# Kernel optimization log

Measured on AMD Instinct MI355X. Metric: run time of the kernel, lower is better.

The kernel has to match this reference:

```python
import jax, jax.numpy as jnp
import numpy as np

B, NVEC, DIM, HEADS, DH, M, ITERS, DEPTH, NCLASS, KER = 8, 4096, 512, 8, 64, 256, 6, 2, 10, 33
INNER = HEADS * DH


def _ln(x, g, b, eps=1e-5):
    mu = x.mean(-1, keepdims=True)
    var = ((x - mu) ** 2).mean(-1, keepdims=True)
    return (x - mu) * jax.lax.rsqrt(var + eps) * g + b


def _mp_pinv(x, iters=ITERS):
    # Moore-Penrose pseudo-inverse via Newton-Schulz iterations (lucidrains).
    # x: [b, h, m, m]
    abs_x = jnp.abs(x)
    col = abs_x.sum(-1).max(-1)  # [b, h]
    row = abs_x.sum(-2).max(-1)  # [b, h]
    z = jnp.swapaxes(x, -1, -2) / (col * row)[..., None, None]
    I = jnp.eye(x.shape[-1], dtype=x.dtype)
    for _ in range(iters):
        xz = x @ z
        z = 0.25 * z @ (13.0 * I - xz @ (15.0 * I - xz @ (7.0 * I - xz)))
    return z


def _nystrom_attn(x, qkv_w, out_w, out_b, conv_w):
    b, n, _ = x.shape
    qkv = x @ qkv_w  # [b, n, 3*inner]
    q, k, v = jnp.split(qkv, 3, axis=-1)
    to_h = lambda t: t.reshape(b, n, HEADS, DH).transpose(0, 2, 1, 3)  # [b,h,n,dh]
    q, k, v = to_h(q), to_h(k), to_h(v)
    q = q * (DH ** -0.5)

    l = n // M  # tokens per landmark segment (n divisible by M)
    q_l = q.reshape(b, HEADS, M, l, DH).mean(3)  # [b,h,M,dh]
    k_l = k.reshape(b, HEADS, M, l, DH).mean(3)

    attn1 = jax.nn.softmax(jnp.einsum('bhnd,bhmd->bhnm', q, k_l), axis=-1)    # [b,h,n,M]
    attn2 = jax.nn.softmax(jnp.einsum('bhmd,bhld->bhml', q_l, k_l), axis=-1)  # [b,h,M,M]
    attn3 = jax.nn.softmax(jnp.einsum('bhmd,bhnd->bhmn', q_l, k), axis=-1)    # [b,h,M,n]

    out = (attn1 @ _mp_pinv(attn2)) @ (attn3 @ v)  # [b,h,n,dh]

    # residual depthwise conv over sequence dim (kernel 33, groups=heads, no bias)
    out = out + jax.lax.conv_general_dilated(
        v, conv_w, (1, 1), [(KER // 2, KER // 2), (0, 0)],
        dimension_numbers=('NCHW', 'OIHW', 'NCHW'), feature_group_count=HEADS)

    out = out.transpose(0, 2, 1, 3).reshape(b, n, INNER)
    return out @ out_w + out_b


def setup_inputs():
    key = jax.random.key(0)
    ks = jax.random.split(key, 12)
    s = 0.02
    f32 = jnp.float32
    return {
        'x': jax.random.normal(ks[0], (B, NVEC, 2), f32),
        'lin_w': jax.random.normal(ks[1], (2, DIM), f32) * s,
        'lin_b': jnp.zeros((DIM,), f32),
        'ln1_g': jnp.ones((DEPTH, DIM), f32),
        'ln1_b': jnp.zeros((DEPTH, DIM), f32),
        'qkv_w': jax.random.normal(ks[2], (DEPTH, DIM, 3 * INNER), f32) * s,
        'out_w': jax.random.normal(ks[3], (DEPTH, INNER, DIM), f32) * s,
        'out_b': jnp.zeros((DEPTH, DIM), f32),
        'conv_w': jax.random.normal(ks[4], (DEPTH, HEADS, 1, KER, 1), f32) * s,
        'ln2_g': jnp.ones((DEPTH, DIM), f32),
        'ln2_b': jnp.zeros((DEPTH, DIM), f32),
        'ff1_w': jax.random.normal(ks[5], (DEPTH, DIM, 4 * DIM), f32) * s,
        'ff1_b': jnp.zeros((DEPTH, 4 * DIM), f32),
        'ff2_w': jax.random.normal(ks[6], (DEPTH, 4 * DIM, DIM), f32) * s,
        'ff2_b': jnp.zeros((DEPTH, DIM), f32),
        'final_w': jax.random.normal(ks[7], (NVEC * DIM, NCLASS), f32) * s,
        'final_b': jnp.zeros((NCLASS,), f32),
    }


def reference(x, lin_w, lin_b, ln1_g, ln1_b, qkv_w, out_w, out_b, conv_w,
              ln2_g, ln2_b, ff1_w, ff1_b, ff2_w, ff2_b, final_w, final_b):
    h = x @ lin_w + lin_b  # [B, NVEC, DIM]
    for i in range(DEPTH):
        h = h + _nystrom_attn(_ln(h, ln1_g[i], ln1_b[i]), qkv_w[i], out_w[i], out_b[i], conv_w[i])
        z = _ln(h, ln2_g[i], ln2_b[i])
        h = h + (jax.nn.gelu(z @ ff1_w[i] + ff1_b[i]) @ ff2_w[i] + ff2_b[i])
    return h.reshape(h.shape[0], -1) @ final_w + final_b  # [B, NCLASS]
```

## Files before the change

### kernel.cpp

```cpp
#include <hip/hip_runtime.h>
#include <hip/hip_bf16.h>

#define BB_ 8
#define NVEC 4096
#define DIM 512
#define HEADS 8
#define DH 64
#define MM_ 256
#define ITERS 6
#define DEPTH 2
#define NCLASS 10
#define KER 33
#define INNER 512
#define LSEG 16

typedef long long ll;
typedef __bf16 bh16;
typedef __attribute__((ext_vector_type(8))) __bf16 bf16x8;
typedef __attribute__((ext_vector_type(4))) float f32x4;

template<int WR, int WC, bool TRB, bool GELU_ACT, bool RESID, bool BF16OUT, bool DUAL>
__global__ void __launch_bounds__(256)
mgemm_k(const bh16* __restrict__ A, const bh16* __restrict__ B,
        const float* __restrict__ bias, void* __restrict__ Cv, void* __restrict__ C2v,
        int K, int lda, int ldb, int ldc,
        int BI, ll sAo, ll sAi, ll sBo, ll sBi, ll sCo, ll sCi,
        float alpha, float diagv)
{
    constexpr int BM = WR * 64, BN = WC * 64;
    const int bz = blockIdx.z;
    const int bo = bz / BI, bi = bz % BI;
    const bh16* Ab = A + bo * sAo + (ll)bi * sAi;
    const bh16* Bb = B + bo * sBo + (ll)bi * sBi;
    const ll coff = bo * sCo + (ll)bi * sCi;
    const int m0 = blockIdx.y * BM;
    const int n0 = blockIdx.x * BN;
    const int tid = threadIdx.x;
    const int lane = tid & 63;
    const int wave = tid >> 6;
    const int wr = wave / WC, wc = wave % WC;

    __shared__ bh16 Al[BM * 32];
    __shared__ bh16 Bl[BN * 32];

    f32x4 acc[4][4];
#pragma unroll
    for (int i = 0; i < 4; ++i)
#pragma unroll
        for (int j = 0; j < 4; ++j) acc[i][j] = (f32x4){0.f, 0.f, 0.f, 0.f};

    const int srow = tid >> 2;
    const int ssl  = tid & 3;

    const int rsel  = ((lane & 15) >> 1) & 3;
    const int kslot = lane >> 4;

    for (int k0 = 0; k0 < K; k0 += 32) {
        __syncthreads();
#pragma unroll
        for (int i = 0; i < BM / 64; ++i) {
            int row = i * 64 + srow;
            int sl = ssl ^ ((row >> 1) & 3);
            bf16x8 v = *(const bf16x8*)(Ab + (ll)(m0 + row) * lda + k0 + ssl * 8);
            *(bf16x8*)(Al + row * 32 + sl * 8) = v;
        }
        if (!TRB) {
#pragma unroll
            for (int i = 0; i < BN / 64; ++i) {
                int row = i * 64 + srow;
                int sl = ssl ^ ((row >> 1) & 3);
                bf16x8 v = *(const bf16x8*)(Bb + (ll)(n0 + row) * ldb + k0 + ssl * 8);
                *(bf16x8*)(Bl + row * 32 + sl * 8) = v;
            }
        } else {
            const int bk = tid >> 3;
            const int nb0 = (tid & 7) * (BN / 8);
#pragma unroll
            for (int v8 = 0; v8 < BN / 64; ++v8) {
                int nb = nb0 + v8 * 8;
                bf16x8 v = *(const bf16x8*)(Bb + (ll)(k0 + bk) * ldb + n0 + nb);
#pragma unroll
                for (int j = 0; j < 8; ++j) {
                    int n = nb + j;
                    int sl = (bk >> 3) ^ ((n >> 1) & 3);
                    Bl[n * 32 + sl * 8 + (bk & 7)] = v[j];
                }
            }
        }
        __syncthreads();

        bf16x8 af[4], bfr[4];
#pragma unroll
        for (int mi = 0; mi < 4; ++mi) {
            int row = wr * 64 + mi * 16 + (lane & 15);
            af[mi] = *(const bf16x8*)(Al + row * 32 + (kslot ^ rsel) * 8);
        }
#pragma unroll
        for (int ni = 0; ni < 4; ++ni) {
            int row = wc * 64 + ni * 16 + (lane & 15);
            bfr[ni] = *(const bf16x8*)(Bl + row * 32 + (kslot ^ rsel) * 8);
        }
#pragma unroll
        for (int mi = 0; mi < 4; ++mi)
#pragma unroll
            for (int ni = 0; ni < 4; ++ni)
                acc[mi][ni] = __builtin_amdgcn_mfma_f32_16x16x32_bf16(
                    af[mi], bfr[ni], acc[mi][ni], 0, 0, 0);
    }

#pragma unroll
    for (int mi = 0; mi < 4; ++mi) {
#pragma unroll
        for (int ni = 0; ni < 4; ++ni) {
            const int colg = n0 + wc * 64 + ni * 16 + (lane & 15);
            const float bia = (!DUAL && bias) ? bias[colg] : 0.f;
#pragma unroll
            for (int r = 0; r < 4; ++r) {
                const int rowg = m0 + wr * 64 + mi * 16 + (lane >> 4) * 4 + r;
                const float a = acc[mi][ni][r];
                const ll off = coff + (ll)rowg * ldc + colg;
                if (DUAL) {
                    ((bh16*)Cv)[off] = (bh16)a;
                    float w = ((rowg == colg) ? diagv : 0.f) - a;
                    ((bh16*)C2v)[off] = (bh16)w;
                } else {
                    float v = alpha * a + bia;
                    if (diagv != 0.f && rowg == colg) v += diagv;
                    if (GELU_ACT) {
                        float t = tanhf(0.7978845608f * (v + 0.044715f * v * v * v));
                        v = 0.5f * v * (1.0f + t);
                    }
                    if (BF16OUT) {
                        ((bh16*)Cv)[off] = (bh16)v;
                    } else {
                        float* p = (float*)Cv + off;
                        float o = v;
                        if (RESID) o += *p;
                        *p = o;
                    }
                }
            }
        }
    }
}

template<int WR, int WC, bool TRB, bool G, bool R, bool BO, bool D>
static inline void mg(hipStream_t s, int M, int N, int K,
                      const bh16* A, int lda, const bh16* B, int ldb,
                      void* C, int ldc, void* C2, const float* bias,
                      int batch, int BI,
                      ll sAo, ll sAi, ll sBo, ll sBi, ll sCo, ll sCi,
                      float alpha, float diagv)
{
    dim3 grid(N / (WC * 64), M / (WR * 64), batch);
    hipLaunchKernelGGL((mgemm_k<WR, WC, TRB, G, R, BO, D>), grid, dim3(256), 0, s,
                       A, B, bias, C, C2, K, lda, ldb, ldc, BI,
                       sAo, sAi, sBo, sBi, sCo, sCi, alpha, diagv);
}

__global__ void embed_k(const float* __restrict__ x, const float* __restrict__ w,
                        const float* __restrict__ b, float* __restrict__ h)
{
    ll idx = (ll)blockIdx.x * 256 + threadIdx.x;
    int d = (int)(idx & 511);
    ll bn = idx >> 9;
    h[idx] = x[bn * 2] * w[d] + x[bn * 2 + 1] * w[512 + d] + b[d];
}

__global__ void __launch_bounds__(256)
ln_k(const float* __restrict__ X, const float* __restrict__ g,
     const float* __restrict__ bta, bh16* __restrict__ Y)
{
    const ll row = blockIdx.x;
    const float* x = X + row * 512;
    bh16* y = Y + row * 512;
    const int tid = threadIdx.x;
    float v0 = x[tid], v1 = x[tid + 256];
    float s = v0 + v1;
    float q = v0 * v0 + v1 * v1;
    __shared__ float sred[8];
    for (int o = 32; o; o >>= 1) { s += __shfl_down(s, o); q += __shfl_down(q, o); }
    const int lane = tid & 63, w = tid >> 6;
    if (lane == 0) { sred[w] = s; sred[4 + w] = q; }
    __syncthreads();
    float ssum = sred[0] + sred[1] + sred[2] + sred[3];
    float qsum = sred[4] + sred[5] + sred[6] + sred[7];
    float mu = ssum * (1.0f / 512.0f);
    float var = qsum * (1.0f / 512.0f) - mu * mu;
    float r = rsqrtf(var + 1e-5f);
    y[tid] = (bh16)((v0 - mu) * r * g[tid] + bta[tid]);
    y[tid + 256] = (bh16)((v1 - mu) * r * g[tid + 256] + bta[tid + 256]);
}

__global__ void cvtT_k(const float* __restrict__ in, bh16* __restrict__ outp, int C, int R)
{
    int idx = blockIdx.x * 256 + threadIdx.x;
    int c = idx % C, rg = idx / C;
    bf16x8 o;
#pragma unroll
    for (int j = 0; j < 8; ++j) o[j] = (bh16)in[(ll)(rg * 8 + j) * C + c];
    *(bf16x8*)(outp + (ll)c * R + rg * 8) = o;
}

__global__ void landmarks_k(const bh16* __restrict__ qkv,
                            bh16* __restrict__ qlb, bh16* __restrict__ klb)
{
    int idx = blockIdx.x * 256 + threadIdx.x;
    int d = idx & 63;
    int m = (idx >> 6) & 255;
    int h = (idx >> 14) & 7;
    int b = idx >> 17;
    const bh16* base = qkv + (ll)b * (NVEC * 1536) + (ll)(m * LSEG) * 1536 + h * 64 + d;
    float sq = 0.f, sk = 0.f;
#pragma unroll
    for (int l = 0; l < LSEG; ++l) {
        sq += (float)base[(ll)l * 1536];
        sk += (float)base[(ll)l * 1536 + 512];
    }
    ll o = (ll)(b * 8 + h) * 16384 + m * 64 + d;
    qlb[o] = (bh16)(sq * (0.0625f * 0.125f));
    klb[o] = (bh16)(sk * 0.0625f);
}

__global__ void wbt_k(const bh16* __restrict__ wb, bh16* __restrict__ wbt)
{
    int idx = blockIdx.x * 256 + threadIdx.x;
    int d = idx & 63, kg = (idx >> 6) & 31, bhh = idx >> 11;
    const bh16* p = wb + (ll)bhh * 16384 + kg * 8 * 64 + d;
    bf16x8 o;
#pragma unroll
    for (int j = 0; j < 8; ++j) o[j] = p[j * 64];
    *(bf16x8*)(wbt + (ll)bhh * 16384 + d * 256 + kg * 8) = o;
}

__global__ void a3vred_k(const float* __restrict__ part, bh16* __restrict__ outp)
{
    int idx = blockIdx.x * 256 + threadIdx.x;
    int smp = idx >> 17;
    int rest = idx & 131071;
    int h = rest >> 14, o = rest & 16383;
    const float* p = part + (ll)smp * 1048576 + (ll)h * 131072 + o;
    float s = 0.f;
#pragma unroll
    for (int j = 0; j < 8; ++j) s += p[j * 16384];
    outp[(ll)(smp * 8 + h) * 16384 + o] = (bh16)s;
}

__global__ void __launch_bounds__(256)
conv_k(const bh16* __restrict__ qkv, const float* __restrict__ cw,
       bh16* __restrict__ convo)
{
    int idx = blockIdx.x * 256 + threadIdx.x;
    int c8 = idx & 63;
    int ng = (idx >> 6) & 1023;
    int b  = idx >> 16;
    const int n0 = ng * 4;
    const int h = c8 >> 3;
    const bh16* v = qkv + (ll)b * (NVEC * 1536) + 1024 + c8 * 8;

    float wreg[KER];
#pragma unroll
    for (int k = 0; k < KER; ++k) wreg[k] = cw[h * KER + k];

    float acc[4][8];
#pragma unroll
    for (int t = 0; t < 4; ++t)
#pragma unroll
        for (int e = 0; e < 8; ++e) acc[t][e] = 0.f;

#pragma unroll
    for (int m = 0; m < 36; ++m) {
        int nn = n0 + m - (KER / 2);
        bf16x8 vv = {};
        if ((unsigned)nn < (unsigned)NVEC)
            vv = *(const bf16x8*)(v + (ll)nn * 1536);
#pragma unroll
        for (int t = 0; t < 4; ++t) {
            constexpr int KMAX = KER - 1;
            int k = m - t;
            if (k >= 0 && k <= KMAX) {
                float wk = wreg[k];
#pragma unroll
                for (int e = 0; e < 8; ++e)
                    acc[t][e] = fmaf((float)vv[e], wk, acc[t][e]);
            }
        }
    }

    bh16* o = convo + (ll)b * (NVEC * 512) + (ll)n0 * 512 + c8 * 8;
#pragma unroll
    for (int t = 0; t < 4; ++t) {
        bf16x8 ov;
#pragma unroll
        for (int e = 0; e < 8; ++e) ov[e] = (bh16)acc[t][e];
        *(bf16x8*)(o + (ll)t * 512) = ov;
    }
}

__device__ __forceinline__ float blkmax(float m, float* red, int tid)
{
#pragma unroll
    for (int o = 32; o; o >>= 1) m = fmaxf(m, __shfl_down(m, o));
    if ((tid & 63) == 0) red[tid >> 6] = m;
    __syncthreads();
    m = fmaxf(fmaxf(red[0], red[1]), fmaxf(red[2], red[3]));
    __syncthreads();
    return m;
}
__device__ __forceinline__ float blksum(float s, float* red, int tid)
{
#pragma unroll
    for (int o = 32; o; o >>= 1) s += __shfl_down(s, o);
    if ((tid & 63) == 0) red[tid >> 6] = s;
    __syncthreads();
    s = red[0] + red[1] + red[2] + red[3];
    __syncthreads();
    return s;
}

__global__ void __launch_bounds__(256)
softmax_bf_k(bh16* __restrict__ X, int L)
{
    const ll row = blockIdx.x;
    bh16* x = X + row * (ll)L;
    const int tid = threadIdx.x;
    __shared__ float red[4];
    float v[16];
    bf16x8 a = *(const bf16x8*)(x + tid * 8);
    bf16x8 b = *(const bf16x8*)(x + 2048 + tid * 8);
#pragma unroll
    for (int j = 0; j < 8; ++j) { v[j] = (float)a[j]; v[8 + j] = (float)b[j]; }
    float m = -1e30f;
#pragma unroll
    for (int j = 0; j < 16; ++j) m = fmaxf(m, v[j]);
    m = blkmax(m, red, tid);
    float s = 0.f;
#pragma unroll
    for (int j = 0; j < 16; ++j) { v[j] = __expf(v[j] - m); s += v[j]; }
    s = blksum(s, red, tid);
    float inv = 1.0f / s;
    bf16x8 oa, ob;
#pragma unroll
    for (int j = 0; j < 8; ++j) { oa[j] = (bh16)(v[j] * inv); ob[j] = (bh16)(v[8 + j] * inv); }
    *(bf16x8*)(x + tid * 8) = oa;
    *(bf16x8*)(x + 2048 + tid * 8) = ob;
}

__global__ void __launch_bounds__(256)
softmax256_k(bh16* __restrict__ X)
{
    const int tid = threadIdx.x;
    const ll row = (ll)blockIdx.x * 8 + (tid >> 5);
    const int l = tid & 31;
    bh16* x = X + row * 256 + l * 8;
    bf16x8 a = *(const bf16x8*)x;
    float v[8];
#pragma unroll
    for (int j = 0; j < 8; ++j) v[j] = (float)a[j];
    float m = -1e30f;
#pragma unroll
    for (int j = 0; j < 8; ++j) m = fmaxf(m, v[j]);
#pragma unroll
    for (int o = 16; o; o >>= 1) m = fmaxf(m, __shfl_xor(m, o, 32));
    float s = 0.f;
#pragma unroll
    for (int j = 0; j < 8; ++j) { v[j] = __expf(v[j] - m); s += v[j]; }
#pragma unroll
    for (int o = 16; o; o >>= 1) s += __shfl_xor(s, o, 32);
    float inv = 1.0f / s;
    bf16x8 ov;
#pragma unroll
    for (int j = 0; j < 8; ++j) ov[j] = (bh16)(v[j] * inv);
    *(bf16x8*)x = ov;
}

__global__ void __launch_bounds__(256)
pinv_init_k(const bh16* __restrict__ X, bh16* __restrict__ Z)
{
    const ll bh = blockIdx.x;
    const bh16* x = X + bh * 65536;
    bh16* z = Z + bh * 65536;
    const int tid = threadIdx.x;
    float rs = 0.f, cs = 0.f;
    for (int j = 0; j < 256; ++j) {
        rs += fabsf((float)x[tid * 256 + j]);
        cs += fabsf((float)x[j * 256 + tid]);
    }
    __shared__ float rbuf[256], cbuf[256];
    rbuf[tid] = rs; cbuf[tid] = cs;
    __syncthreads();
    for (int o = 128; o; o >>= 1) {
        if (tid < o) {
            rbuf[tid] = fmaxf(rbuf[tid], rbuf[tid + o]);
            cbuf[tid] = fmaxf(cbuf[tid], cbuf[tid + o]);
        }
        __syncthreads();
    }
    float inv = 1.0f / (rbuf[0] * cbuf[0]);
    for (int e = tid; e < 65536; e += 256) {
        int i = e >> 8, j = e & 255;
        z[e] = (bh16)((float)x[j * 256 + i] * inv);
    }
}

__global__ void final_init_k(const float* __restrict__ fb, float* __restrict__ out)
{
    int i = threadIdx.x;
    if (i < BB_ * NCLASS) out[i] = fb[i % NCLASS];
}

__global__ void __launch_bounds__(256)
final_gemv_k(const float* __restrict__ hbuf, const float* __restrict__ w,
             float* __restrict__ out)
{
    const int b = blockIdx.y;
    const int chunk = blockIdx.x;
    const int tid = threadIdx.x;
    const float* hrow = hbuf + (ll)b * (NVEC * DIM);
    float pc[NCLASS] = {};
    const int k0 = chunk * 8192;
    for (int e = 0; e < 32; ++e) {
        int k = k0 + e * 256 + tid;
        float hv = hrow[k];
        const float* wr = w + (ll)k * NCLASS;
#pragma unroll
        for (int c = 0; c < NCLASS; ++c) pc[c] += hv * wr[c];
    }
    __shared__ float red[256];
    for (int c = 0; c < NCLASS; ++c) {
        red[tid] = pc[c];
        __syncthreads();
        for (int o = 128; o; o >>= 1) {
            if (tid < o) red[tid] += red[tid + o];
            __syncthreads();
        }
        if (tid == 0) atomicAdd(out + b * NCLASS + c, red[0]);
        __syncthreads();
    }
}

extern "C" void kernel_launch(void* const* d_in, const int* in_sizes, int n_in,
                              void* d_out, int out_size, void* d_ws, size_t ws_size,
                              hipStream_t stream)
{
    const float* x      = (const float*)d_in[0];
    const float* lin_w  = (const float*)d_in[1];
    const float* lin_b  = (const float*)d_in[2];
    const float* ln1_g  = (const float*)d_in[3];
    const float* ln1_b  = (const float*)d_in[4];
    const float* qkv_w  = (const float*)d_in[5];
    const float* out_w  = (const float*)d_in[6];
    const float* out_b  = (const float*)d_in[7];
    const float* conv_w = (const float*)d_in[8];
    const float* ln2_g  = (const float*)d_in[9];
    const float* ln2_b  = (const float*)d_in[10];
    const float* ff1_w  = (const float*)d_in[11];
    const float* ff1_b  = (const float*)d_in[12];
    const float* ff2_w  = (const float*)d_in[13];
    const float* ff2_b  = (const float*)d_in[14];
    const float* final_w = (const float*)d_in[15];
    const float* final_b = (const float*)d_in[16];
    float* out = (float*)d_out;
    float* ws  = (float*)d_ws;

    float* H    = ws;
    bh16*  QKV  = (bh16*)(ws + 16777216);
    float* P    = ws + 41943040;
    bh16*  qlbf = (bh16*)(ws + 52428800);
    bh16*  klbf = (bh16*)(ws + 52953088);
    bh16*  A3Vb = (bh16*)(ws + 53477376);
    bh16*  WBb  = (bh16*)(ws + 54001664);
    bh16*  WBT  = (bh16*)(ws + 54525952);
    bh16*  WQT  = (bh16*)(ws + 55050240);
    bh16*  WOT  = (bh16*)(ws + 55443456);
    bh16*  F1WT = (bh16*)(ws + 55574528);
    bh16*  F2WT = (bh16*)(ws + 56098816);
    if (ws_size < 56623104ULL * 4) return;

    bh16*  XLNall = (bh16*)P;
    bh16*  ATT3c  = (bh16*)P;
    float* A3Vp   = P + 8388608;
    bh16*  CONVa  = (bh16*)P;
    bh16*  Xbf = (bh16*)P;
    bh16*  Z0  = (bh16*)(P + 2097152);
    bh16*  Z1  = (bh16*)(P + 4194304);
    bh16*  T1  = (bh16*)(P + 6291456);
    bh16*  T2  = (bh16*)(P + 8388608);
    bh16*  ATT1c  = (bh16*)P;
    bh16*  AOUTc  = (bh16*)(P + 8388608);
    bh16*  XLNc   = (bh16*)P;
    bh16*  HIDc   = (bh16*)(P + 2097152);

    const ll SMP = (ll)NVEC * 1536;

    hipLaunchKernelGGL(embed_k, dim3(65536), dim3(256), 0, stream, x, lin_w, lin_b, H);

    for (int i = 0; i < DEPTH; ++i) {
        const float* wq  = qkv_w + (ll)i * 512 * 1536;
        const float* wo  = out_w + (ll)i * 512 * 512;
        const float* bo  = out_b + (ll)i * 512;
        const float* cw  = conv_w + (ll)i * HEADS * KER;
        const float* g1  = ln1_g + (ll)i * 512;
        const float* b1  = ln1_b + (ll)i * 512;
        const float* g2  = ln2_g + (ll)i * 512;
        const float* b2  = ln2_b + (ll)i * 512;
        const float* f1w = ff1_w + (ll)i * 512 * 2048;
        const float* f1b = ff1_b + (ll)i * 2048;
        const float* f2w = ff2_w + (ll)i * 2048 * 512;
        const float* f2b = ff2_b + (ll)i * 512;

        hipLaunchKernelGGL(cvtT_k, dim3(384), dim3(256), 0, stream, wq, WQT, 1536, 512);
        hipLaunchKernelGGL(cvtT_k, dim3(128), dim3(256), 0, stream, wo, WOT, 512, 512);
        hipLaunchKernelGGL(cvtT_k, dim3(512), dim3(256), 0, stream, f1w, F1WT, 2048, 512);
        hipLaunchKernelGGL(cvtT_k, dim3(512), dim3(256), 0, stream, f2w, F2WT, 512, 2048);

        hipLaunchKernelGGL(ln_k, dim3(32768), dim3(256), 0, stream, H, g1, b1, XLNall);
        mg<2,2,0,0,0,1,0>(stream, 32768, 1536, 512, XLNall, 512, WQT, 512,
            QKV, 1536, nullptr, nullptr, 1, 1, 0,0, 0,0, 0,0, 1.f, 0.f);

        hipLaunchKernelGGL(landmarks_k, dim3(4096), dim3(256), 0, stream, QKV, qlbf, klbf);

        for (int c = 0; c < 4; ++c) {
            const bh16* qkvc = QKV + (ll)c * 2 * SMP;
            mg<2,2,0,0,0,1,0>(stream, 256, 4096, 64,
                qlbf + (ll)c * 262144, 64, qkvc + 512, 1536,
                ATT3c, 4096, nullptr, nullptr, 16, 8,
                131072, 16384, SMP, 64, 8388608LL, 1048576, 1.f, 0.f);
            hipLaunchKernelGGL(softmax_bf_k, dim3(4096), dim3(256), 0, stream, ATT3c, 4096);
            for (int s = 0; s < 2; ++s) {
                mg<4,1,1,0,0,0,0>(stream, 256, 64, 512,
                    ATT3c + (ll)s * 8 * 1048576, 4096, qkvc + (ll)s * SMP + 1024, 1536,
                    A3Vp + (ll)s * 1048576, 64, nullptr, nullptr, 64, 8,
                    1048576, 512, 64, 512LL * 1536, 131072, 16384, 1.f, 0.f);
            }
            hipLaunchKernelGGL(a3vred_k, dim3(1024), dim3(256), 0, stream,
                               A3Vp, A3Vb + (ll)c * 2 * 131072);
        }

        hipLaunchKernelGGL(conv_k, dim3(2048), dim3(256), 0, stream, QKV, cw, CONVa);
        mg<2,2,0,0,1,0,0>(stream, 32768, 512, 512, CONVa, 512, WOT, 512,
            H, 512, nullptr, nullptr, 1, 1, 0,0, 0,0, 0,0, 1.f, 0.f);

        mg<2,2,0,0,0,1,0>(stream, 256, 256, 64, qlbf, 64, klbf, 64,
            Xbf, 256, nullptr, nullptr, 64, 64, 0, 16384, 0, 16384, 0, 65536, 1.f, 0.f);
        hipLaunchKernelGGL(softmax256_k, dim3(2048), dim3(256), 0, stream, Xbf);
        hipLaunchKernelGGL(pinv_init_k, dim3(64), dim3(256), 0, stream, Xbf, Z0);
        bh16* zc = Z0; bh16* zn = Z1;
        for (int it = 0; it < ITERS; ++it) {
            mg<2,2,1,0,0,1,1>(stream, 256, 256, 256, Xbf, 256, zc, 256,
                T1, 256, T2, nullptr, 64, 64, 0, 65536, 0, 65536, 0, 65536, 1.f, 7.f);
            mg<2,2,1,0,0,1,0>(stream, 256, 256, 256, T1, 256, T2, 256,
                zn, 256, nullptr, nullptr, 64, 64, 0, 65536, 0, 65536, 0, 65536, -1.f, 15.f);
            mg<2,2,1,0,0,1,0>(stream, 256, 256, 256, T1, 256, zn, 256,
                T2, 256, nullptr, nullptr, 64, 64, 0, 65536, 0, 65536, 0, 65536, -1.f, 13.f);
            mg<2,2,1,0,0,1,0>(stream, 256, 256, 256, zc, 256, T2, 256,
                zn, 256, nullptr, nullptr, 64, 64, 0, 65536, 0, 65536, 0, 65536, 0.25f, 0.f);
            bh16* t = zc; zc = zn; zn = t;
        }
        mg<4,1,1,0,0,1,0>(stream, 256, 64, 256, zc, 256, A3Vb, 64,
            WBb, 64, nullptr, nullptr, 64, 64, 0, 65536, 0, 16384, 0, 16384, 1.f, 0.f);
        hipLaunchKernelGGL(wbt_k, dim3(512), dim3(256), 0, stream, WBb, WBT);

        for (int c = 0; c < 4; ++c) {
            const bh16* qkvc = QKV + (ll)c * 2 * SMP;
            mg<2,2,0,0,0,1,0>(stream, 4096, 256, 64,
                qkvc, 1536, klbf + (ll)c * 262144, 64,
                ATT1c, 256, nullptr, nullptr, 16, 8,
                SMP, 64, 131072, 16384, 8388608LL, 1048576, 0.125f, 0.f);
            hipLaunchKernelGGL(softmax256_k, dim3(8192), dim3(256), 0, stream, ATT1c);
            mg<4,1,0,0,0,1,0>(stream, 4096, 64, 256,
                ATT1c, 256, WBT + (ll)c * 262144, 256,
                AOUTc, 512, nullptr, nullptr, 16, 8,
                8388608LL, 1048576, 131072, 16384, 2097152LL, 64, 1.f, 0.f);
            mg<2,2,0,0,1,0,0>(stream, 8192, 512, 512, AOUTc, 512, WOT, 512,
                H + (ll)c * 2 * 2097152, 512, nullptr, bo, 1, 1, 0,0, 0,0, 0,0, 1.f, 0.f);
        }

        for (int c = 0; c < 4; ++c) {
            float* Hc = H + (ll)c * 2 * 2097152;
            hipLaunchKernelGGL(ln_k, dim3(8192), dim3(256), 0, stream, Hc, g2, b2, XLNc);
            mg<2,2,0,1,0,1,0>(stream, 8192, 2048, 512, XLNc, 512, F1WT, 512,
                HIDc, 2048, nullptr, f1b, 1, 1, 0,0, 0,0, 0,0, 1.f, 0.f);
            mg<2,2,0,0,1,0,0>(stream, 8192, 512, 2048, HIDc, 2048, F2WT, 2048,
                Hc, 512, nullptr, f2b, 1, 1, 0,0, 0,0, 0,0, 1.f, 0.f);
        }
    }

    hipLaunchKernelGGL(final_init_k, dim3(1), dim3(128), 0, stream, final_b, out);
    hipLaunchKernelGGL(final_gemv_k, dim3(256, BB_), dim3(256), 0, stream, H, final_w, out);
}
```

Measured before the change: 3.670 ms.

## Use direct global-to-LDS loads in GEMM, tile weight transpose, batch final GEMV

The GEMM A/B tile loads now go through global_load_lds, which writes straight into LDS instead of staging in registers. The swizzle moves from the LDS address to the global address to keep the same layout. The weight transpose-convert kernel now uses a 64x64 shared-memory tile so both its reads and writes are coalesced. The final GEMV handles four batch rows per block to reuse each weight load, and reduces with wave shuffles instead of a shared-memory tree. The direct-to-LDS path depends on the builtin's per-lane addressing matching the swizzled layout, so a mismatch would corrupt results.

```diff
diff --git a/kernel.cpp b/kernel.cpp
--- a/kernel.cpp
+++ b/kernel.cpp
@@ -60,17 +60,25 @@
 #pragma unroll
         for (int i = 0; i < BM / 64; ++i) {
             int row = i * 64 + srow;
-            int sl = ssl ^ ((row >> 1) & 3);
-            bf16x8 v = *(const bf16x8*)(Ab + (ll)(m0 + row) * lda + k0 + ssl * 8);
-            *(bf16x8*)(Al + row * 32 + sl * 8) = v;
+            int gsl = ssl ^ ((row >> 1) & 3);
+            __builtin_amdgcn_global_load_lds(
+                (const __attribute__((address_space(1))) unsigned int*)
+                    (Ab + (ll)(m0 + row) * lda + k0 + gsl * 8),
+                (__attribute__((address_space(3))) unsigned int*)
+                    (Al + row * 32 + ssl * 8),
+                16, 0, 0);
         }
         if (!TRB) {
 #pragma unroll
             for (int i = 0; i < BN / 64; ++i) {
                 int row = i * 64 + srow;
-                int sl = ssl ^ ((row >> 1) & 3);
-                bf16x8 v = *(const bf16x8*)(Bb + (ll)(n0 + row) * ldb + k0 + ssl * 8);
-                *(bf16x8*)(Bl + row * 32 + sl * 8) = v;
+                int gsl = ssl ^ ((row >> 1) & 3);
+                __builtin_amdgcn_global_load_lds(
+                    (const __attribute__((address_space(1))) unsigned int*)
+                        (Bb + (ll)(n0 + row) * ldb + k0 + gsl * 8),
+                    (__attribute__((address_space(3))) unsigned int*)
+                        (Bl + row * 32 + ssl * 8),
+                    16, 0, 0);
             }
         } else {
             const int bk = tid >> 3;
@@ -192,14 +200,30 @@
     y[tid + 256] = (bh16)((v1 - mu) * r * g[tid + 256] + bta[tid + 256]);
 }
 
-__global__ void cvtT_k(const float* __restrict__ in, bh16* __restrict__ outp, int C, int R)
-{
-    int idx = blockIdx.x * 256 + threadIdx.x;
-    int c = idx % C, rg = idx / C;
-    bf16x8 o;
-#pragma unroll
-    for (int j = 0; j < 8; ++j) o[j] = (bh16)in[(ll)(rg * 8 + j) * C + c];
-    *(bf16x8*)(outp + (ll)c * R + rg * 8) = o;
+__global__ void __launch_bounds__(256)
+cvtT_k(const float* __restrict__ in, bh16* __restrict__ outp, int C, int R)
+{
+    __shared__ float t[64][65];
+    const int nCt = C >> 6;
+    const int c0 = (blockIdx.x % nCt) * 64;
+    const int r0 = (blockIdx.x / nCt) * 64;
+    const int tid = threadIdx.x;
+#pragma unroll
+    for (int j = 0; j < 16; ++j) {
+        int idx = j * 256 + tid;
+        int lr = idx >> 6, lc = idx & 63;
+        t[lc][lr] = in[(ll)(r0 + lr) * C + c0 + lc];
+    }
+    __syncthreads();
+#pragma unroll
+    for (int v = 0; v < 2; ++v) {
+        int flat = v * 256 + tid;
+        int lc = flat >> 3, r8 = (flat & 7) * 8;
+        bf16x8 o;
+#pragma unroll
+        for (int j = 0; j < 8; ++j) o[j] = (bh16)t[lc][r8 + j];
+        *(bf16x8*)(outp + (ll)(c0 + lc) * R + r0 + r8) = o;
+    }
 }
 
 __global__ void landmarks_k(const bh16* __restrict__ qkv,
@@ -413,29 +437,40 @@
 final_gemv_k(const float* __restrict__ hbuf, const float* __restrict__ w,
              float* __restrict__ out)
 {
-    const int b = blockIdx.y;
+    const int half = blockIdx.y;
     const int chunk = blockIdx.x;
     const int tid = threadIdx.x;
-    const float* hrow = hbuf + (ll)b * (NVEC * DIM);
-    float pc[NCLASS] = {};
     const int k0 = chunk * 8192;
+    float pc[4][NCLASS] = {};
     for (int e = 0; e < 32; ++e) {
         int k = k0 + e * 256 + tid;
-        float hv = hrow[k];
         const float* wr = w + (ll)k * NCLASS;
-#pragma unroll
-        for (int c = 0; c < NCLASS; ++c) pc[c] += hv * wr[c];
-    }
-    __shared__ float red[256];
-    for (int c = 0; c < NCLASS; ++c) {
-        red[tid] = pc[c];
-        __syncthreads();
-        for (int o = 128; o; o >>= 1) {
-            if (tid < o) red[tid] += red[tid + o];
-            __syncthreads();
-        }
-        if (tid == 0) atomicAdd(out + b * NCLASS + c, red[0]);
-        __syncthreads();
+        float wv[NCLASS];
+#pragma unroll
+        for (int c = 0; c < NCLASS; ++c) wv[c] = wr[c];
+#pragma unroll
+        for (int b = 0; b < 4; ++b) {
+            float hv = hbuf[(ll)(half * 4 + b) * (NVEC * DIM) + k];
+#pragma unroll
+            for (int c = 0; c < NCLASS; ++c) pc[b][c] = fmaf(hv, wv[c], pc[b][c]);
+        }
+    }
+    __shared__ float red[4][4][NCLASS];
+    const int lane = tid & 63, wv_ = tid >> 6;
+#pragma unroll
+    for (int b = 0; b < 4; ++b)
+#pragma unroll
+        for (int c = 0; c < NCLASS; ++c) {
+            float s = pc[b][c];
+#pragma unroll
+            for (int o = 32; o; o >>= 1) s += __shfl_down(s, o);
+            if (lane == 0) red[wv_][b][c] = s;
+        }
+    __syncthreads();
+    if (tid < 4 * NCLASS) {
+        int b = tid / NCLASS, c = tid % NCLASS;
+        float s = red[0][b][c] + red[1][b][c] + red[2][b][c] + red[3][b][c];
+        atomicAdd(out + (half * 4 + b) * NCLASS + c, s);
     }
 }
 
@@ -509,10 +544,10 @@
         const float* f2w = ff2_w + (ll)i * 2048 * 512;
         const float* f2b = ff2_b + (ll)i * 512;
 
-        hipLaunchKernelGGL(cvtT_k, dim3(384), dim3(256), 0, stream, wq, WQT, 1536, 512);
-        hipLaunchKernelGGL(cvtT_k, dim3(128), dim3(256), 0, stream, wo, WOT, 512, 512);
-        hipLaunchKernelGGL(cvtT_k, dim3(512), dim3(256), 0, stream, f1w, F1WT, 2048, 512);
-        hipLaunchKernelGGL(cvtT_k, dim3(512), dim3(256), 0, stream, f2w, F2WT, 512, 2048);
+        hipLaunchKernelGGL(cvtT_k, dim3(192), dim3(256), 0, stream, wq, WQT, 1536, 512);
+        hipLaunchKernelGGL(cvtT_k, dim3(64), dim3(256), 0, stream, wo, WOT, 512, 512);
+        hipLaunchKernelGGL(cvtT_k, dim3(256), dim3(256), 0, stream, f1w, F1WT, 2048, 512);
+        hipLaunchKernelGGL(cvtT_k, dim3(256), dim3(256), 0, stream, f2w, F2WT, 512, 2048);
 
         hipLaunchKernelGGL(ln_k, dim3(32768), dim3(256), 0, stream, H, g1, b1, XLNall);
         mg<2,2,0,0,0,1,0>(stream, 32768, 1536, 512, XLNall, 512, WQT, 512,
@@ -587,5 +622,5 @@
     }
 
     hipLaunchKernelGGL(final_init_k, dim3(1), dim3(128), 0, stream, final_b, out);
-    hipLaunchKernelGGL(final_gemv_k, dim3(256, BB_), dim3(256), 0, stream, H, final_w, out);
-}
+    hipLaunchKernelGGL(final_gemv_k, dim3(256, 2), dim3(256), 0, stream, H, final_w, out);
+}
```

Result: faster. 3.526 ms (-3.9%).
